# Performance work log

Measured on AMD Instinct MI355X. Metric: run time of the kernel, lower is better.

Reference implementation:

```python
import jax, jax.numpy as jnp
import numpy as np

NEG_BIG = -9e15
ALPHA = 0.2  # LeakyReLU negative slope


def setup_inputs() -> dict:
    key = jax.random.key(0)
    k1, k2, k3, k4 = jax.random.split(key, 4)
    N, F_in, F_out = 8192, 256, 64
    inp = jax.random.normal(k1, (N, F_in), dtype=jnp.float32)
    adj = jax.random.randint(k2, (N, N), 0, 2, dtype=jnp.int32)
    W = jax.random.normal(k3, (F_in, F_out), dtype=jnp.float32) * 0.05
    a = jax.random.normal(k4, (2 * F_out, 1), dtype=jnp.float32) * 0.05
    return {"input": inp, "adj": adj, "W": W, "a": a}


def reference(input, adj, W, a):
    # h = X W : [N, F_out]
    h = input @ W
    F_out = W.shape[1]
    # a_input[i,j] = concat(h_i, h_j); a_input @ a = h@a1 broadcast over j + h@a2 broadcast over i.
    a1 = a[:F_out, 0]   # [F_out]
    a2 = a[F_out:, 0]   # [F_out]
    s1 = h @ a1         # [N]
    s2 = h @ a2         # [N]
    e = jax.nn.leaky_relu(s1[:, None] + s2[None, :], negative_slope=ALPHA)  # [N, N]
    att = jnp.where(adj > 0, e, jnp.float32(NEG_BIG))
    att = jax.nn.softmax(att, axis=1)
    # dropout is identity in eval mode (training=False)
    h_prime = att @ h   # [N, F_out]
    return jax.nn.elu(h_prime)
```

## Files before the change

kernel.cpp:

```cpp
#include <hip/hip_runtime.h>
#include <hip/hip_bf16.h>

typedef __bf16 bf16_t;
typedef __attribute__((ext_vector_type(8))) __bf16 bf16x8;
typedef __attribute__((ext_vector_type(4))) __bf16 bf16x4;
typedef __attribute__((ext_vector_type(4))) float floatx4;
typedef __attribute__((ext_vector_type(4))) int intx4;

#define NN 8192
#define FIN 256
#define FOUT 64
#define GAT_ALPHA 0.2f
#define NSLICE 4
#define JS (NN / NSLICE)
#define JCH 128
#define NCH (JS / JCH)
#define IB 64

typedef const __attribute__((address_space(1))) void gv_t;
typedef __attribute__((address_space(3))) void lv_t;
#define GLOAD16(gp, lp) \
    __builtin_amdgcn_global_load_lds((gv_t*)(gp), (lv_t*)(lp), 16, 0, 0)

__global__ __launch_bounds__(256) void gat_h_kernel(
    const float* __restrict__ input,
    const float* __restrict__ W,
    const float* __restrict__ a,
    bf16_t* __restrict__ hTf,
    float* __restrict__ e1g, float* __restrict__ f1g,
    float* __restrict__ e2g, float* __restrict__ f2g)
{
    alignas(16) __shared__ bf16_t in_lds[32][264];
    alignas(16) __shared__ bf16_t wt_lds[64][264];
    __shared__ float h_lds[32][65];

    const int t  = threadIdx.x;
    const int i0 = blockIdx.x * 32;

    #pragma unroll
    for (int v = 0; v < 8; v++) {
        int u  = v * 256 + t;
        int i  = u >> 6;
        int k4 = (u & 63) * 4;
        floatx4 x = *(const floatx4*)(input + (size_t)(i0 + i) * FIN + k4);
        bf16x4 b;
        #pragma unroll
        for (int e = 0; e < 4; e++) b[e] = (bf16_t)x[e];
        *(bf16x4*)(&in_lds[i][k4]) = b;
    }
    #pragma unroll
    for (int v = 0; v < 16; v++) {
        int u  = v * 256 + t;
        int k  = u >> 4;
        int f4 = (u & 15) * 4;
        floatx4 wv = *(const floatx4*)(W + k * FOUT + f4);
        #pragma unroll
        for (int e = 0; e < 4; e++) wt_lds[f4 + e][k] = (bf16_t)wv[e];
    }
    __syncthreads();

    const int wave = t >> 6;
    const int lane = t & 63;
    const int i16  = (wave & 1) * 16;
    const int f32  = (wave >> 1) * 32;
    const int lm   = lane & 15;
    const int lq   = lane >> 4;

    floatx4 acc0 = {0.f, 0.f, 0.f, 0.f};
    floatx4 acc1 = {0.f, 0.f, 0.f, 0.f};
    #pragma unroll
    for (int ks = 0; ks < 8; ks++) {
        int ko = ks * 32 + lq * 8;
        bf16x8 af = *(const bf16x8*)(&in_lds[i16 + lm][ko]);
        bf16x8 b0 = *(const bf16x8*)(&wt_lds[f32 + lm][ko]);
        bf16x8 b1 = *(const bf16x8*)(&wt_lds[f32 + 16 + lm][ko]);
        acc0 = __builtin_amdgcn_mfma_f32_16x16x32_bf16(af, b0, acc0, 0, 0, 0);
        acc1 = __builtin_amdgcn_mfma_f32_16x16x32_bf16(af, b1, acc1, 0, 0, 0);
    }

    {
        const int jb  = i0 >> 5;
        const int lqp = (i16 >> 3) + (lq >> 1);
        const int e0  = (lq & 1) * 4;
        #pragma unroll
        for (int c = 0; c < 2; c++) {
            floatx4 acc = c ? acc1 : acc0;
            int ft = (f32 >> 4) + c;
            bf16x4 hp;
            #pragma unroll
            for (int r = 0; r < 4; r++) hp[r] = (bf16_t)acc[r];
            *(bf16x4*)(hTf + (size_t)(((jb * 4 + ft) * 64 + lqp * 16 + lm) * 8 + e0)) = hp;
        }
    }
    #pragma unroll
    for (int c = 0; c < 2; c++) {
        floatx4 acc = c ? acc1 : acc0;
        #pragma unroll
        for (int r = 0; r < 4; r++)
            h_lds[i16 + lq * 4 + r][f32 + c * 16 + lm] = acc[r];
    }
    __syncthreads();

    if (t < 64) {
        int r   = t & 31;
        int sel = t >> 5;
        const float* av = a + sel * FOUT;
        float s = 0.f;
        #pragma unroll 8
        for (int f = 0; f < FOUT; f++) s += h_lds[r][f] * av[f];
        int gi = i0 + r;
        float E = expf(s);
        float F = expf(GAT_ALPHA * s);
        if (sel == 0) { e1g[gi] = E; f1g[gi] = F; }
        else          { e2g[gi] = E; f2g[gi] = F; }
    }
}

__global__ __launch_bounds__(256, 2) void gat_att_kernel(
    const int* __restrict__ adj,
    const bf16_t* __restrict__ hTf,
    const float* __restrict__ e1g, const float* __restrict__ f1g,
    const float* __restrict__ e2g, const float* __restrict__ f2g,
    float* __restrict__ pacc,
    float* __restrict__ prs)
{
    __shared__ int   adjL[2][IB][JCH];
    __shared__ float e2l[JS], f2l[JS];

    const int t     = threadIdx.x;
    const int i0    = blockIdx.x * IB;
    const int slice = blockIdx.y;
    const int jbase = slice * JS;

    const int wave = t >> 6;
    const int lane = t & 63;
    const int lm   = lane & 15;
    const int lq   = lane >> 4;

    {
        int o = wave * 512;
        GLOAD16(e2g + jbase + o + lane * 4,       e2l + o);
        GLOAD16(e2g + jbase + o + 256 + lane * 4, e2l + o + 256);
        GLOAD16(f2g + jbase + o + lane * 4,       f2l + o);
        GLOAD16(f2g + jbase + o + 256 + lane * 4, f2l + o + 256);
    }

    auto stage = [&](int b, int c) {
        const int jg = jbase + c * JCH;
        #pragma unroll
        for (int h = 0; h < 8; h++) {
            int r0 = wave * 16 + h * 2;
            int r  = r0 + (lane >> 5);
            int g  = (lane & 31) ^ (r & 7);
            GLOAD16(adj + (size_t)(i0 + r) * NN + jg + g * 4, &adjL[b][r0][0]);
        }
    };

    stage(0, 0);

    const int   row = i0 + wave * 16 + lm;
    const float E1  = e1g[row];
    const float F1  = f1g[row];

    floatx4 acc0 = {0.f,0.f,0.f,0.f}, acc1 = {0.f,0.f,0.f,0.f};
    floatx4 acc2 = {0.f,0.f,0.f,0.f}, acc3 = {0.f,0.f,0.f,0.f};
    floatx4 accR = {0.f,0.f,0.f,0.f};
    bf16x8 ones;
    #pragma unroll
    for (int e = 0; e < 8; e++) ones[e] = (bf16_t)1.0f;

    for (int c = 0; c < NCH; c++) {
        if (c + 1 < NCH) {
            stage((c + 1) & 1, c + 1);
            asm volatile("s_waitcnt vmcnt(8)" ::: "memory");
        } else {
            asm volatile("s_waitcnt vmcnt(0)" ::: "memory");
        }
        __builtin_amdgcn_s_barrier();
        asm volatile("" ::: "memory");

        const char* aB = (const char*)&adjL[c & 1][wave * 16 + lm][0];
        #pragma unroll
        for (int ks = 0; ks < 4; ks++) {
            int g0 = ks * 8 + lq * 2;
            intx4 a0 = *(const intx4*)(aB + (((g0    ) ^ (lm & 7)) << 4));
            intx4 a1 = *(const intx4*)(aB + (((g0 + 1) ^ (lm & 7)) << 4));
            int jo = c * JCH + ks * 32 + lq * 8;
            floatx4 e2a = *(const floatx4*)(&e2l[jo]);
            floatx4 e2b = *(const floatx4*)(&e2l[jo + 4]);
            floatx4 f2a = *(const floatx4*)(&f2l[jo]);
            floatx4 f2b = *(const floatx4*)(&f2l[jo + 4]);
            bf16x8 frag;
            #pragma unroll
            for (int e = 0; e < 4; e++) {
                float w0 = fmaxf(E1 * e2a[e], F1 * f2a[e]);
                frag[e]     = (bf16_t)((a0[e] > 0) ? w0 : 0.f);
                float w1 = fmaxf(E1 * e2b[e], F1 * f2b[e]);
                frag[e + 4] = (bf16_t)((a1[e] > 0) ? w1 : 0.f);
            }
            const int jb = slice * (JS / 32) + c * 4 + ks;
            const bf16_t* hb = hTf + (size_t)jb * 2048 + (size_t)lane * 8;
            bf16x8 b0 = *(const bf16x8*)(hb);
            bf16x8 b1 = *(const bf16x8*)(hb + 512);
            bf16x8 b2 = *(const bf16x8*)(hb + 1024);
            bf16x8 b3 = *(const bf16x8*)(hb + 1536);
            acc0 = __builtin_amdgcn_mfma_f32_16x16x32_bf16(frag, b0, acc0, 0, 0, 0);
            acc1 = __builtin_amdgcn_mfma_f32_16x16x32_bf16(frag, b1, acc1, 0, 0, 0);
            acc2 = __builtin_amdgcn_mfma_f32_16x16x32_bf16(frag, b2, acc2, 0, 0, 0);
            acc3 = __builtin_amdgcn_mfma_f32_16x16x32_bf16(frag, b3, acc3, 0, 0, 0);
            accR = __builtin_amdgcn_mfma_f32_16x16x32_bf16(frag, ones, accR, 0, 0, 0);
        }

        asm volatile("" ::: "memory");
        __builtin_amdgcn_s_barrier();
        asm volatile("" ::: "memory");
    }

    if (lm == 0) {
        #pragma unroll
        for (int r = 0; r < 4; r++)
            prs[(size_t)slice * NN + i0 + wave * 16 + lq * 4 + r] = accR[r];
    }

    float* pa = pacc + (size_t)slice * NN * FOUT
                     + (size_t)(i0 + wave * 16) * FOUT;
    #pragma unroll
    for (int ft = 0; ft < 4; ft++) {
        floatx4 acc = (ft == 0) ? acc0 : (ft == 1) ? acc1
                    : (ft == 2) ? acc2 : acc3;
        #pragma unroll
        for (int r = 0; r < 4; r++)
            pa[(size_t)(lq * 4 + r) * FOUT + ft * 16 + lm] = acc[r];
    }
}

__global__ __launch_bounds__(256) void gat_combine_kernel(
    const float* __restrict__ pacc,
    const float* __restrict__ prs,
    float* __restrict__ out)
{
    int idx = blockIdx.x * 256 + threadIdx.x;
    int i   = idx >> 4;
    floatx4 s = {0.f, 0.f, 0.f, 0.f};
    float rs  = 0.f;
    #pragma unroll
    for (int p = 0; p < NSLICE; p++) {
        floatx4 v = *(const floatx4*)(pacc + (size_t)p * NN * FOUT + (size_t)idx * 4);
        s += v;
        rs += prs[p * NN + i];
    }
    float rinv = (rs > 0.f) ? 1.0f / rs : 0.f;
    floatx4 r;
    #pragma unroll
    for (int e = 0; e < 4; e++) {
        float x = s[e] * rinv;
        r[e] = (x > 0.f) ? x : (expf(x) - 1.0f);
    }
    *(floatx4*)(out + (size_t)idx * 4) = r;
}

extern "C" void kernel_launch(void* const* d_in, const int* in_sizes, int n_in,
                              void* d_out, int out_size, void* d_ws, size_t ws_size,
                              hipStream_t stream) {
    const float* input = (const float*)d_in[0];
    const int*   adj   = (const int*)d_in[1];
    const float* W     = (const float*)d_in[2];
    const float* a     = (const float*)d_in[3];
    float*       out   = (float*)d_out;

    char* ws = (char*)d_ws;
    bf16_t* hTf = (bf16_t*)ws;
    float*  e1g = (float*)(ws + (1 << 20));
    float*  f1g = e1g + NN;
    float*  e2g = f1g + NN;
    float*  f2g = e2g + NN;
    float*  pacc = f2g + NN;
    float*  prs  = pacc + (size_t)NSLICE * NN * FOUT;

    gat_h_kernel<<<NN / 32, 256, 0, stream>>>(input, W, a, hTf,
                                              e1g, f1g, e2g, f2g);
    dim3 gridB(NN / IB, NSLICE);
    gat_att_kernel<<<gridB, 256, 0, stream>>>(adj, hTf, e1g, f1g, e2g, f2g,
                                              pacc, prs);
    gat_combine_kernel<<<NN * FOUT / 4 / 256, 256, 0, stream>>>(pacc, prs, out);
}
```

Baseline: 393.1 us.

## Pack adjacency into bitmask in a pre-pass and double slice count

Adds a separate kernel that reads the int32 adjacency matrix once and packs it into a 1-bit-per-entry bitmask. The attention kernel then loads a small bitmask tile per block instead of streaming int32 adjacency chunks, which removes the double-buffered staging loop and its per-chunk barriers. The number of j-slices goes from 4 to 8 and occupancy hints are raised to raise parallelism. The full adjacency read still happens, now in the pack kernel, and this adds a kernel launch, a bitmask write/read round trip, and more partial-sum traffic for the combine stage.

```diff
diff --git a/kernel.cpp b/kernel.cpp
--- a/kernel.cpp
+++ b/kernel.cpp
@@ -11,10 +11,9 @@
 #define FIN 256
 #define FOUT 64
 #define GAT_ALPHA 0.2f
-#define NSLICE 4
+#define NSLICE 8
 #define JS (NN / NSLICE)
-#define JCH 128
-#define NCH (JS / JCH)
+#define NJB (JS / 32)
 #define IB 64
 
 typedef const __attribute__((address_space(1))) void gv_t;
@@ -116,15 +115,41 @@
     }
 }
 
-__global__ __launch_bounds__(256, 2) void gat_att_kernel(
+__global__ __launch_bounds__(256) void gat_pack_kernel(
     const int* __restrict__ adj,
+    unsigned long long* __restrict__ bits)
+{
+    const int tid = blockIdx.x * 256 + threadIdx.x;
+    const int r   = tid >> 7;
+    const int c   = tid & 127;
+    const int* src = adj + (size_t)r * NN + c * 64;
+    unsigned int lo = 0, hi = 0;
+    #pragma unroll
+    for (int u = 0; u < 8; u++) {
+        intx4 v = *(const intx4*)(src + u * 4);
+        #pragma unroll
+        for (int e = 0; e < 4; e++)
+            lo |= (v[e] > 0 ? 1u : 0u) << (u * 4 + e);
+    }
+    #pragma unroll
+    for (int u = 0; u < 8; u++) {
+        intx4 v = *(const intx4*)(src + 32 + u * 4);
+        #pragma unroll
+        for (int e = 0; e < 4; e++)
+            hi |= (v[e] > 0 ? 1u : 0u) << (u * 4 + e);
+    }
+    bits[(size_t)r * 128 + c] = ((unsigned long long)hi << 32) | lo;
+}
+
+__global__ __launch_bounds__(256, 4) void gat_att_kernel(
+    const unsigned char* __restrict__ bits,
     const bf16_t* __restrict__ hTf,
     const float* __restrict__ e1g, const float* __restrict__ f1g,
     const float* __restrict__ e2g, const float* __restrict__ f2g,
     float* __restrict__ pacc,
     float* __restrict__ prs)
 {
-    __shared__ int   adjL[2][IB][JCH];
+    __shared__ unsigned char bitsL[IB][128];
     __shared__ float e2l[JS], f2l[JS];
 
     const int t     = threadIdx.x;
@@ -137,30 +162,24 @@
     const int lm   = lane & 15;
     const int lq   = lane >> 4;
 
+    #pragma unroll
+    for (int h = 0; h < 2; h++) {
+        int r0 = wave * 16 + h * 8;
+        int r  = r0 + (lane >> 3);
+        int g  = (lane & 7) ^ (r & 7);
+        GLOAD16(bits + (size_t)(i0 + r) * 1024 + slice * 128 + g * 16,
+                &bitsL[r0][0]);
+    }
     {
-        int o = wave * 512;
-        GLOAD16(e2g + jbase + o + lane * 4,       e2l + o);
-        GLOAD16(e2g + jbase + o + 256 + lane * 4, e2l + o + 256);
-        GLOAD16(f2g + jbase + o + lane * 4,       f2l + o);
-        GLOAD16(f2g + jbase + o + 256 + lane * 4, f2l + o + 256);
-    }
-
-    auto stage = [&](int b, int c) {
-        const int jg = jbase + c * JCH;
-        #pragma unroll
-        for (int h = 0; h < 8; h++) {
-            int r0 = wave * 16 + h * 2;
-            int r  = r0 + (lane >> 5);
-            int g  = (lane & 31) ^ (r & 7);
-            GLOAD16(adj + (size_t)(i0 + r) * NN + jg + g * 4, &adjL[b][r0][0]);
-        }
-    };
-
-    stage(0, 0);
-
-    const int   row = i0 + wave * 16 + lm;
-    const float E1  = e1g[row];
-    const float F1  = f1g[row];
+        int o = wave * 256;
+        GLOAD16(e2g + jbase + o + lane * 4, e2l + o);
+        GLOAD16(f2g + jbase + o + lane * 4, f2l + o);
+    }
+    __syncthreads();
+
+    const int   row = wave * 16 + lm;
+    const float E1  = e1g[i0 + row];
+    const float F1  = f1g[i0 + row];
 
     floatx4 acc0 = {0.f,0.f,0.f,0.f}, acc1 = {0.f,0.f,0.f,0.f};
     floatx4 acc2 = {0.f,0.f,0.f,0.f}, acc3 = {0.f,0.f,0.f,0.f};
@@ -169,51 +188,38 @@
     #pragma unroll
     for (int e = 0; e < 8; e++) ones[e] = (bf16_t)1.0f;
 
-    for (int c = 0; c < NCH; c++) {
-        if (c + 1 < NCH) {
-            stage((c + 1) & 1, c + 1);
-            asm volatile("s_waitcnt vmcnt(8)" ::: "memory");
-        } else {
-            asm volatile("s_waitcnt vmcnt(0)" ::: "memory");
+    const bf16_t* hslice = hTf + (size_t)slice * NJB * 2048 + (size_t)lane * 8;
+
+    #pragma unroll 8
+    for (int jb = 0; jb < NJB; jb++) {
+        int off = (((jb >> 2) ^ (row & 7)) << 4) | ((jb & 3) << 2);
+        int wrd = *(const int*)(&bitsL[row][off]);
+        unsigned bt = ((unsigned)wrd >> (lq * 8)) & 0xffu;
+
+        int jo = jb * 32 + lq * 8;
+        floatx4 e2a = *(const floatx4*)(&e2l[jo]);
+        floatx4 e2b = *(const floatx4*)(&e2l[jo + 4]);
+        floatx4 f2a = *(const floatx4*)(&f2l[jo]);
+        floatx4 f2b = *(const floatx4*)(&f2l[jo + 4]);
+        bf16x8 frag;
+        #pragma unroll
+        for (int e = 0; e < 4; e++) {
+            float w0 = fmaxf(E1 * e2a[e], F1 * f2a[e]);
+            frag[e]     = (bt & (1u << e))       ? (bf16_t)w0 : (bf16_t)0.f;
+            float w1 = fmaxf(E1 * e2b[e], F1 * f2b[e]);
+            frag[e + 4] = (bt & (1u << (e + 4))) ? (bf16_t)w1 : (bf16_t)0.f;
         }
-        __builtin_amdgcn_s_barrier();
-        asm volatile("" ::: "memory");
-
-        const char* aB = (const char*)&adjL[c & 1][wave * 16 + lm][0];
-        #pragma unroll
-        for (int ks = 0; ks < 4; ks++) {
-            int g0 = ks * 8 + lq * 2;
-            intx4 a0 = *(const intx4*)(aB + (((g0    ) ^ (lm & 7)) << 4));
-            intx4 a1 = *(const intx4*)(aB + (((g0 + 1) ^ (lm & 7)) << 4));
-            int jo = c * JCH + ks * 32 + lq * 8;
-            floatx4 e2a = *(const floatx4*)(&e2l[jo]);
-            floatx4 e2b = *(const floatx4*)(&e2l[jo + 4]);
-            floatx4 f2a = *(const floatx4*)(&f2l[jo]);
-            floatx4 f2b = *(const floatx4*)(&f2l[jo + 4]);
-            bf16x8 frag;
-            #pragma unroll
-            for (int e = 0; e < 4; e++) {
-                float w0 = fmaxf(E1 * e2a[e], F1 * f2a[e]);
-                frag[e]     = (bf16_t)((a0[e] > 0) ? w0 : 0.f);
-                float w1 = fmaxf(E1 * e2b[e], F1 * f2b[e]);
-                frag[e + 4] = (bf16_t)((a1[e] > 0) ? w1 : 0.f);
-            }
-            const int jb = slice * (JS / 32) + c * 4 + ks;
-            const bf16_t* hb = hTf + (size_t)jb * 2048 + (size_t)lane * 8;
-            bf16x8 b0 = *(const bf16x8*)(hb);
-            bf16x8 b1 = *(const bf16x8*)(hb + 512);
-            bf16x8 b2 = *(const bf16x8*)(hb + 1024);
-            bf16x8 b3 = *(const bf16x8*)(hb + 1536);
-            acc0 = __builtin_amdgcn_mfma_f32_16x16x32_bf16(frag, b0, acc0, 0, 0, 0);
-            acc1 = __builtin_amdgcn_mfma_f32_16x16x32_bf16(frag, b1, acc1, 0, 0, 0);
-            acc2 = __builtin_amdgcn_mfma_f32_16x16x32_bf16(frag, b2, acc2, 0, 0, 0);
-            acc3 = __builtin_amdgcn_mfma_f32_16x16x32_bf16(frag, b3, acc3, 0, 0, 0);
-            accR = __builtin_amdgcn_mfma_f32_16x16x32_bf16(frag, ones, accR, 0, 0, 0);
-        }
-
-        asm volatile("" ::: "memory");
-        __builtin_amdgcn_s_barrier();
-        asm volatile("" ::: "memory");
+
+        const bf16_t* hb = hslice + (size_t)jb * 2048;
+        bf16x8 b0 = *(const bf16x8*)(hb);
+        bf16x8 b1 = *(const bf16x8*)(hb + 512);
+        bf16x8 b2 = *(const bf16x8*)(hb + 1024);
+        bf16x8 b3 = *(const bf16x8*)(hb + 1536);
+        acc0 = __builtin_amdgcn_mfma_f32_16x16x32_bf16(frag, b0, acc0, 0, 0, 0);
+        acc1 = __builtin_amdgcn_mfma_f32_16x16x32_bf16(frag, b1, acc1, 0, 0, 0);
+        acc2 = __builtin_amdgcn_mfma_f32_16x16x32_bf16(frag, b2, acc2, 0, 0, 0);
+        acc3 = __builtin_amdgcn_mfma_f32_16x16x32_bf16(frag, b3, acc3, 0, 0, 0);
+        accR = __builtin_amdgcn_mfma_f32_16x16x32_bf16(frag, ones, accR, 0, 0, 0);
     }
 
     if (lm == 0) {
@@ -274,13 +280,15 @@
     float*  f1g = e1g + NN;
     float*  e2g = f1g + NN;
     float*  f2g = e2g + NN;
-    float*  pacc = f2g + NN;
+    unsigned long long* bitsw = (unsigned long long*)(f2g + NN);
+    float*  pacc = (float*)((char*)bitsw + NN * 128 * 8);
     float*  prs  = pacc + (size_t)NSLICE * NN * FOUT;
 
+    gat_pack_kernel<<<NN * NN / 64 / 256, 256, 0, stream>>>(adj, bitsw);
     gat_h_kernel<<<NN / 32, 256, 0, stream>>>(input, W, a, hTf,
                                               e1g, f1g, e2g, f2g);
     dim3 gridB(NN / IB, NSLICE);
-    gat_att_kernel<<<gridB, 256, 0, stream>>>(adj, hTf, e1g, f1g, e2g, f2g,
-                                              pacc, prs);
+    gat_att_kernel<<<gridB, 256, 0, stream>>>((const unsigned char*)bitsw, hTf,
+                                              e1g, f1g, e2g, f2g, pacc, prs);
     gat_combine_kernel<<<NN * FOUT / 4 / 256, 256, 0, stream>>>(pacc, prs, out);
 }
```

Measured after the change: 406.8 us. 3.5% more time.
